# Optimization experiments

Hardware: AMD Instinct MI355X
Metric: run time of the kernel (lower is better)

Reference implementation:

```python
import jax, jax.numpy as jnp
import numpy as np

B, N, D_VIS, D_LBL = 64, 256, 2048, 512
H, F_OUT = 8, 256            # n_heads, gat_out_per_head_dim
D_IN = D_VIS + D_LBL         # 2560, GAT input dim
D_GAT = H * F_OUT            # 2048, concat-heads output dim
D_EMB = 512                  # final_embedding_dim
ALPHA = 0.2                  # LeakyReLU negative slope


def setup_inputs() -> dict:
    key = jax.random.key(0)
    ks = jax.random.split(key, 9)
    visual_features = jax.random.normal(ks[0], (B, D_VIS), jnp.float32)
    labels_features = jax.random.normal(ks[1], (N, D_LBL), jnp.float32)
    adj = (jax.random.uniform(ks[2], (N, N)) < 0.1).astype(jnp.float32)
    label_adj_matrix = jnp.maximum(adj, jnp.eye(N, dtype=jnp.float32))
    s = 1.0 / np.sqrt(D_IN)
    W_gat = jax.random.uniform(ks[3], (D_IN, H, F_OUT), jnp.float32, -s, s)
    a_src = jax.random.uniform(ks[4], (H, F_OUT), jnp.float32, -s, s)
    a_dst = jax.random.uniform(ks[5], (H, F_OUT), jnp.float32, -s, s)
    sg = 1.0 / np.sqrt(D_GAT)
    pool_q = jax.random.uniform(ks[6], (D_GAT,), jnp.float32, -sg, sg)
    fc_W = jax.random.uniform(ks[7], (D_GAT, D_EMB), jnp.float32, -sg, sg)
    fc_b = jax.random.uniform(ks[8], (D_EMB,), jnp.float32, -sg, sg)
    return {"visual_features": visual_features, "labels_features": labels_features,
            "label_adj_matrix": label_adj_matrix, "W_gat": W_gat, "a_src": a_src,
            "a_dst": a_dst, "pool_q": pool_q, "fc_W": fc_W, "fc_b": fc_b}


def reference(visual_features, labels_features, label_adj_matrix,
              W_gat, a_src, a_dst, pool_q, fc_W, fc_b):
    # Build per-sample contextualized label node features: (B, N, D_IN)
    x = jnp.concatenate(
        [jnp.broadcast_to(labels_features[None], (B, N, D_LBL)),
         jnp.broadcast_to(visual_features[:, None, :], (B, N, D_VIS))], axis=-1)
    # Multi-head GAT layer, batched over B (the torch code loops over B)
    Wh = jnp.einsum('bnd,dhf->bnhf', x, W_gat)            # (B, N, H, F)
    src = jnp.einsum('bnhf,hf->bhn', Wh, a_src)           # (B, H, N)
    dst = jnp.einsum('bnhf,hf->bhn', Wh, a_dst)           # (B, H, N)
    e = src[:, :, :, None] + dst[:, :, None, :]           # (B, H, N, N)
    e = jnp.where(e > 0, e, ALPHA * e)                    # LeakyReLU
    mask = (label_adj_matrix > 0)[None, None]             # (1, 1, N, N)
    scores = jnp.where(mask, e, jnp.float32(-9e15))
    attn = jax.nn.softmax(scores, axis=-1)                # (B, H, N, N)
    out = jnp.einsum('bhij,bjhf->bihf', attn, Wh)         # (B, N, H, F)
    out = jax.nn.elu(out.reshape(B, N, D_GAT))            # concat heads + ELU
    # attention pooling over label nodes
    pw = jax.nn.softmax(jnp.einsum('bnd,d->bn', out, pool_q), axis=-1)
    pooled = jnp.einsum('bn,bnd->bd', pw, out)            # (B, D_GAT)
    return pooled @ fc_W + fc_b                           # (B, D_EMB)
```

## Files before the change

kernel.cpp:

```cpp
#include <hip/hip_runtime.h>
#include <hip/hip_bf16.h>
#include <math.h>

#define BB 64
#define NN 256
#define D_VIS 2048
#define D_LBL 512
#define HH 8
#define FF 256
#define DG 2048
#define DE 512
#define ALPHA 0.2f
#define PSTRIDE 264
#define NSPLIT 4

using bf16 = __hip_bfloat16;
using short8 = __attribute__((ext_vector_type(8))) short;
using f32x4  = __attribute__((ext_vector_type(4))) float;
__device__ __forceinline__ float b2f(bf16 x) { return __bfloat162float(x); }
__device__ __forceinline__ unsigned short f2bs(float x) {
    bf16 h = __float2bfloat16(x);
    unsigned short u;
    __builtin_memcpy(&u, &h, 2);
    return u;
}
__device__ __forceinline__ float bs2f(unsigned short u) {
    unsigned int x = (unsigned int)u << 16;
    float f;
    __builtin_memcpy(&f, &x, 4);
    return f;
}

__global__ void __launch_bounds__(256) k_wh(const float* __restrict__ labels,
                                            const float* __restrict__ visual,
                                            const float* __restrict__ Wg,
                                            unsigned short* __restrict__ WhLbT,
                                            float* __restrict__ WhVz,
                                            const float* __restrict__ aSrc,
                                            const float* __restrict__ aDst,
                                            float* __restrict__ srcLp,
                                            float* __restrict__ dstLp,
                                            float* __restrict__ srcVp,
                                            float* __restrict__ dstVp,
                                            const float* __restrict__ adj,
                                            unsigned short* __restrict__ abits) {
    const int t = threadIdx.x;
    const int y = blockIdx.y;
    if (y == 8) {
        if (t < 128) {
            const int r = t >> 4, s = t & 15;
            const int i = blockIdx.x * 8 + r;
            unsigned int bits = 0;
#pragma unroll
            for (int jj = 0; jj < 8; ++jj) {
                const float2 av = *(const float2*)(adj + (size_t)i * NN + 2 * s + 32 * jj);
                bits |= (av.x > 0.f ? 1u : 0u) << (2 * jj);
                bits |= (av.y > 0.f ? 1u : 0u) << (2 * jj + 1);
            }
            abits[i * 16 + s] = (unsigned short)bits;
        }
        return;
    }

    __shared__ unsigned short As[2][64][72];
    __shared__ unsigned short Bs[2][64][72];
    const int w = t >> 6;
    const int lane = t & 63;
    const int l15 = lane & 15, quad = lane >> 4;
    const int n0 = blockIdx.x * 64;
    const int p2 = blockIdx.x & 3;
    const bool isL = (y < 4);
    const int m0  = isL ? y * 64 : 0;
    const int z   = isL ? 0 : (y - 4);
    const int kb0 = z * 512;
    const float* A = isL ? labels : visual;
    const int lda  = isL ? D_LBL : D_VIS;
    const float* Wb = Wg + (isL ? 0 : (size_t)D_LBL * DG);

    f32x4 acc[4];
#pragma unroll
    for (int mi = 0; mi < 4; ++mi) acc[mi] = (f32x4){0.f, 0.f, 0.f, 0.f};

    float4 ra[4], rb[4];
    auto load_tile = [&](int kc) {
        const int kb = kb0 + kc * 64;
#pragma unroll
        for (int p = 0; p < 4; ++p) {
            const int idx = t + 256 * p;
            const int r = idx >> 4, q4 = idx & 15;
            ra[p] = *(const float4*)(A + (size_t)(m0 + r) * lda + kb + 4 * q4);
        }
#pragma unroll
        for (int p = 0; p < 4; ++p) {
            const int kk = (t >> 4) + 16 * p;
            const int c4 = (t & 15) * 4;
            rb[p] = *(const float4*)(Wb + (size_t)(kb + kk) * DG + n0 + c4);
        }
    };
    auto store_tile = [&](int buf) {
#pragma unroll
        for (int p = 0; p < 4; ++p) {
            const int idx = t + 256 * p;
            const int r = idx >> 4, q4 = idx & 15;
            unsigned short s4[4] = {f2bs(ra[p].x), f2bs(ra[p].y), f2bs(ra[p].z), f2bs(ra[p].w)};
            __builtin_memcpy(&As[buf][r][4 * q4], s4, 8);
        }
#pragma unroll
        for (int p = 0; p < 4; ++p) {
            const int kk = (t >> 4) + 16 * p;
            const int c4 = (t & 15) * 4;
            Bs[buf][c4 + 0][kk] = f2bs(rb[p].x);
            Bs[buf][c4 + 1][kk] = f2bs(rb[p].y);
            Bs[buf][c4 + 2][kk] = f2bs(rb[p].z);
            Bs[buf][c4 + 3][kk] = f2bs(rb[p].w);
        }
    };

    load_tile(0);
    store_tile(0);
    __syncthreads();
    for (int kc = 0; kc < 8; ++kc) {
        const int cur = kc & 1;
        if (kc < 7) load_tile(kc + 1);
#pragma unroll
        for (int ks = 0; ks < 2; ++ks) {
            const short8 bf = *(const short8*)&Bs[cur][w * 16 + l15][ks * 32 + quad * 8];
#pragma unroll
            for (int mi = 0; mi < 4; ++mi) {
                const short8 af = *(const short8*)&As[cur][mi * 16 + l15][ks * 32 + quad * 8];
                acc[mi] = __builtin_amdgcn_mfma_f32_16x16x32_bf16(af, bf, acc[mi], 0, 0, 0);
            }
        }
        if (kc < 7) store_tile(cur ^ 1);
        __syncthreads();
    }
    const int col = n0 + w * 16 + l15;
    const int h = col >> 8;
    const float as = aSrc[col], ad = aDst[col];
    if (isL) {
#pragma unroll
        for (int mi = 0; mi < 4; ++mi) {
            unsigned short s4[4];
#pragma unroll
            for (int r = 0; r < 4; ++r) s4[r] = f2bs(acc[mi][r]);
            __builtin_memcpy(&WhLbT[(size_t)col * NN + m0 + mi * 16 + quad * 4], s4, 8);
        }
#pragma unroll
        for (int mi = 0; mi < 4; ++mi)
#pragma unroll
            for (int r = 0; r < 4; ++r) {
                float sv = acc[mi][r] * as;
                float dv = acc[mi][r] * ad;
#pragma unroll
                for (int off = 1; off < 16; off <<= 1) {
                    sv += __shfl_xor(sv, off);
                    dv += __shfl_xor(dv, off);
                }
                if (l15 == 0) {
                    const int row = m0 + mi * 16 + quad * 4 + r;
                    srcLp[(p2 * NN + row) * HH + h] = sv;
                    dstLp[(p2 * NN + row) * HH + h] = dv;
                }
            }
    } else {
        float* Wv = WhVz + (size_t)z * BB * DG;
#pragma unroll
        for (int mi = 0; mi < 4; ++mi)
#pragma unroll
            for (int r = 0; r < 4; ++r)
                Wv[(size_t)(mi * 16 + quad * 4 + r) * DG + col] = acc[mi][r];
        const int pv = p2 * 4 + z;
#pragma unroll
        for (int mi = 0; mi < 4; ++mi)
#pragma unroll
            for (int r = 0; r < 4; ++r) {
                float sv = acc[mi][r] * as;
                float dv = acc[mi][r] * ad;
#pragma unroll
                for (int off = 1; off < 16; off <<= 1) {
                    sv += __shfl_xor(sv, off);
                    dv += __shfl_xor(dv, off);
                }
                if (l15 == 0) {
                    const int row = mi * 16 + quad * 4 + r;
                    srcVp[(pv * BB + row) * HH + h] = sv;
                    dstVp[(pv * BB + row) * HH + h] = dv;
                }
            }
    }
}

__global__ void __launch_bounds__(512, 4) k_gat(const unsigned short* __restrict__ WhLbT,
                                                const float* __restrict__ WhVz,
                                                const float* __restrict__ srcLp,
                                                const float* __restrict__ dstLp,
                                                const float* __restrict__ srcVp,
                                                const float* __restrict__ dstVp,
                                                const unsigned short* __restrict__ abits,
                                                const float* __restrict__ pool_q,
                                                bf16* __restrict__ outb,
                                                float* __restrict__ ps_p) {
    const int bid = blockIdx.x;
    const int h = bid & 7;
    const int b = bid >> 3;
    const int t = threadIdx.x;
    const int w = t >> 6;
    const int lane = t & 63;
    const int l15 = lane & 15, quad = lane >> 4;

    __shared__ __align__(16) unsigned short Pl[64][PSTRIDE];
    __shared__ __align__(16) float dls2[2 * NN];
    __shared__ float slsA[NN], slsC[NN], slsTE[NN];
    __shared__ float inv[64];
    __shared__ float psl[8][64];

    if (t < NN) {
        float dl = 0.f, sl = 0.f;
#pragma unroll
        for (int p = 0; p < 4; ++p) {
            dl += dstLp[(p * NN + t) * HH + h];
            sl += srcLp[(p * NN + t) * HH + h];
        }
        dls2[2 * t]     = __expf(dl);
        dls2[2 * t + 1] = __expf(ALPHA * dl);
        float c = 0.f;
#pragma unroll
        for (int p = 0; p < 16; ++p)
            c += srcVp[(p * BB + b) * HH + h] + dstVp[(p * BB + b) * HH + h];
        const float u = c + sl;
        slsA[t]  = __expf(u);
        slsC[t]  = __expf(ALPHA * u);
        slsTE[t] = __expf(-u);
    }
    const int n0 = w * 32;
    float wv[2] = {0.f, 0.f};
#pragma unroll
    for (int z = 0; z < 4; ++z)
#pragma unroll
        for (int ni = 0; ni < 2; ++ni)
            wv[ni] += WhVz[(size_t)z * BB * DG + (size_t)b * DG + h * FF + n0 + ni * 16 + l15];
    const float pqv0 = pool_q[h * FF + n0 + l15];
    const float pqv1 = pool_q[h * FF + n0 + 16 + l15];
    const unsigned short* wb = WhLbT + (size_t)(h * FF + n0 + l15) * NN + quad * 8;
    __syncthreads();

    for (int it = 0; it < 4; ++it) {
        const int i0 = it * 64;

        {
            const int g = lane >> 4, s = lane & 15;
#pragma unroll
            for (int rr = 0; rr < 2; ++rr) {
                const int iloc = w * 8 + rr * 4 + g;
                const int i = i0 + iloc;
                const unsigned int mb = abits[i * 16 + s];
                const float Ai = slsA[i], Ci = slsC[i], TEi = slsTE[i];
                float pr[16];
                float sum = 0.f;
#pragma unroll
                for (int jj = 0; jj < 8; ++jj) {
                    const int j0 = 2 * s + 32 * jj;
                    const float4 bd = *(const float4*)&dls2[2 * j0];
                    const bool g0 = bd.x > TEi;
                    const bool g1 = bd.z > TEi;
                    float p0 = (g0 ? Ai : Ci) * (g0 ? bd.x : bd.y);
                    float p1 = (g1 ? Ai : Ci) * (g1 ? bd.z : bd.w);
                    p0 = (mb & (1u << (2 * jj)))     ? p0 : 0.f;
                    p1 = (mb & (1u << (2 * jj + 1))) ? p1 : 0.f;
                    pr[2 * jj] = p0; pr[2 * jj + 1] = p1;
                    sum += p0 + p1;
                }
#pragma unroll
                for (int off = 1; off < 16; off <<= 1) sum += __shfl_xor(sum, off);
                if (s == 0) inv[iloc] = 1.0f / sum;
#pragma unroll
                for (int jj = 0; jj < 8; ++jj) {
                    const unsigned int pk =
                        ((unsigned int)f2bs(pr[2 * jj + 1]) << 16) | f2bs(pr[2 * jj]);
                    *(unsigned int*)&Pl[iloc][2 * s + 32 * jj] = pk;
                }
            }
        }
        __syncthreads();

        f32x4 acc[4][2];
#pragma unroll
        for (int mi = 0; mi < 4; ++mi)
#pragma unroll
            for (int ni = 0; ni < 2; ++ni) acc[mi][ni] = (f32x4){0.f, 0.f, 0.f, 0.f};

        short8 bc0 = *(const short8*)(wb);
        short8 bc1 = *(const short8*)(wb + (size_t)16 * NN);
#pragma unroll
        for (int kc = 0; kc < 8; ++kc) {
            short8 bn0, bn1;
            if (kc < 7) {
                bn0 = *(const short8*)(wb + (kc + 1) * 32);
                bn1 = *(const short8*)(wb + (size_t)16 * NN + (kc + 1) * 32);
            }
            short8 a[4];
#pragma unroll
            for (int mi = 0; mi < 4; ++mi)
                a[mi] = *(const short8*)&Pl[mi * 16 + l15][kc * 32 + quad * 8];
#pragma unroll
            for (int mi = 0; mi < 4; ++mi)
                acc[mi][0] = __builtin_amdgcn_mfma_f32_16x16x32_bf16(a[mi], bc0, acc[mi][0], 0, 0, 0);
#pragma unroll
            for (int mi = 0; mi < 4; ++mi)
                acc[mi][1] = __builtin_amdgcn_mfma_f32_16x16x32_bf16(a[mi], bc1, acc[mi][1], 0, 0, 0);
            bc0 = bn0; bc1 = bn1;
        }

#pragma unroll
        for (int mi = 0; mi < 4; ++mi)
#pragma unroll
            for (int r = 0; r < 4; ++r) {
                const int row = mi * 16 + quad * 4 + r;
                const float ivr = inv[row];
                bf16* orow = outb + ((size_t)(b * NN + i0 + row)) * DG + h * FF + n0;
                float x0 = fmaf(acc[mi][0][r], ivr, wv[0]);
                float x1 = fmaf(acc[mi][1][r], ivr, wv[1]);
                x0 = x0 > 0.f ? x0 : (__expf(x0) - 1.0f);
                x1 = x1 > 0.f ? x1 : (__expf(x1) - 1.0f);
                orow[l15]      = __float2bfloat16(x0);
                orow[16 + l15] = __float2bfloat16(x1);
                float dot = fmaf(x0, pqv0, x1 * pqv1);
#pragma unroll
                for (int off = 1; off < 16; off <<= 1) dot += __shfl_xor(dot, off);
                if (l15 == 0) psl[w][row] = dot;
            }
        __syncthreads();
        if (t < 64) {
            float s = 0.f;
#pragma unroll
            for (int ww = 0; ww < 8; ++ww) s += psl[ww][t];
            ps_p[((size_t)h * BB + b) * NN + i0 + t] = s;
        }
    }
}

__global__ void __launch_bounds__(256) k_pool(const bf16* __restrict__ outb,
                                              const float* __restrict__ ps_p,
                                              float* __restrict__ pooled_p,
                                              const float* __restrict__ fcb,
                                              float* __restrict__ out) {
    const int dt = blockIdx.x;
    const int b  = blockIdx.y;
    const int ns = blockIdx.z;
    const int t  = threadIdx.x;
    if (dt == 0 && ns == 0) {
        out[b * DE + t]       = fcb[t];
        out[b * DE + 256 + t] = fcb[256 + t];
    }
    __shared__ float wsm[NN];
    __shared__ float redm[4];
    __shared__ float reds[4];
    float v = 0.f;
#pragma unroll
    for (int s = 0; s < 8; ++s)
        v += ps_p[((size_t)s * BB + b) * NN + t];
    float m = v;
#pragma unroll
    for (int off = 32; off; off >>= 1) m = fmaxf(m, __shfl_xor(m, off));
    if ((t & 63) == 0) redm[t >> 6] = m;
    __syncthreads();
    m = fmaxf(fmaxf(redm[0], redm[1]), fmaxf(redm[2], redm[3]));
    const float e = __expf(v - m);
    float s = e;
#pragma unroll
    for (int off = 32; off; off >>= 1) s += __shfl_xor(s, off);
    if ((t & 63) == 0) reds[t >> 6] = s;
    __syncthreads();
    s = reds[0] + reds[1] + reds[2] + reds[3];
    wsm[t] = e / s;
    __syncthreads();
    const int d0 = dt * 512 + t * 2;
    const int nb = ns * 64;
    float a0 = 0.f, a1 = 0.f;
    const bf16* base = outb + (size_t)b * NN * DG + d0;
#pragma unroll 8
    for (int n = 0; n < 64; ++n) {
        unsigned int q = *(const unsigned int*)(base + (size_t)(nb + n) * DG);
        const float wn = wsm[nb + n];
        a0 = fmaf(wn, bs2f((unsigned short)(q & 0xffff)), a0);
        a1 = fmaf(wn, bs2f((unsigned short)(q >> 16)), a1);
    }
    float2 r2 = {a0, a1};
    *(float2*)(pooled_p + ((size_t)(ns * BB + b)) * DG + d0) = r2;
}

__global__ void __launch_bounds__(256) k_mgemm(const float* __restrict__ Ap,
                                               const float* __restrict__ W, int ldw,
                                               float* __restrict__ C, int ldc,
                                               int kSlice, int kIters) {
    __shared__ unsigned short As[32][72];
    __shared__ unsigned short Bs[64][72];
    const int t = threadIdx.x;
    const int w = t >> 6;
    const int lane = t & 63;
    const int l15 = lane & 15, quad = lane >> 4;
    const int n0 = blockIdx.x * 64;
    const int m0 = blockIdx.y * 32;
    const int kb0 = blockIdx.z * kSlice;
    f32x4 acc[2];
    acc[0] = (f32x4){0.f, 0.f, 0.f, 0.f};
    acc[1] = (f32x4){0.f, 0.f, 0.f, 0.f};
    for (int kc = 0; kc < kIters; ++kc) {
        const int kb = kb0 + kc * 64;
#pragma unroll
        for (int p = 0; p < 2; ++p) {
            const int idx = t + 256 * p;
            const int r = idx >> 4, q4 = idx & 15;
            const float* ap = Ap + (size_t)(m0 + r) * DG + kb + 4 * q4;
            const float4 v0 = *(const float4*)(ap);
            const float4 v1 = *(const float4*)(ap + (size_t)BB * DG);
            const float4 v2 = *(const float4*)(ap + (size_t)2 * BB * DG);
            const float4 v3 = *(const float4*)(ap + (size_t)3 * BB * DG);
            const float vx = v0.x + v1.x + v2.x + v3.x;
            const float vy = v0.y + v1.y + v2.y + v3.y;
            const float vz = v0.z + v1.z + v2.z + v3.z;
            const float vw = v0.w + v1.w + v2.w + v3.w;
            unsigned short s4[4] = {f2bs(vx), f2bs(vy), f2bs(vz), f2bs(vw)};
            __builtin_memcpy(&As[r][4 * q4], s4, 8);
        }
#pragma unroll
        for (int p = 0; p < 4; ++p) {
            const int kk = (t >> 4) + 16 * p;
            const int c4 = (t & 15) * 4;
            const float4 v = *(const float4*)(W + (size_t)(kb + kk) * ldw + n0 + c4);
            Bs[c4 + 0][kk] = f2bs(v.x);
            Bs[c4 + 1][kk] = f2bs(v.y);
            Bs[c4 + 2][kk] = f2bs(v.z);
            Bs[c4 + 3][kk] = f2bs(v.w);
        }
        __syncthreads();
#pragma unroll
        for (int ks = 0; ks < 2; ++ks) {
            const short8 bf = *(const short8*)&Bs[w * 16 + l15][ks * 32 + quad * 8];
#pragma unroll
            for (int mi = 0; mi < 2; ++mi) {
                const short8 af = *(const short8*)&As[mi * 16 + l15][ks * 32 + quad * 8];
                acc[mi] = __builtin_amdgcn_mfma_f32_16x16x32_bf16(af, bf, acc[mi], 0, 0, 0);
            }
        }
        __syncthreads();
    }
    const int col = n0 + w * 16 + l15;
#pragma unroll
    for (int mi = 0; mi < 2; ++mi)
#pragma unroll
        for (int r = 0; r < 4; ++r)
            atomicAdd(&C[(size_t)(m0 + mi * 16 + quad * 4 + r) * ldc + col], acc[mi][r]);
}

extern "C" void kernel_launch(void* const* d_in, const int* in_sizes, int n_in,
                              void* d_out, int out_size, void* d_ws, size_t ws_size,
                              hipStream_t stream) {
    (void)in_sizes; (void)n_in; (void)out_size; (void)ws_size;
    const float* visual = (const float*)d_in[0];
    const float* labels = (const float*)d_in[1];
    const float* adj    = (const float*)d_in[2];
    const float* Wg     = (const float*)d_in[3];
    const float* a_src  = (const float*)d_in[4];
    const float* a_dst  = (const float*)d_in[5];
    const float* pool_q = (const float*)d_in[6];
    const float* fcW    = (const float*)d_in[7];
    const float* fcb    = (const float*)d_in[8];
    float* out = (float*)d_out;

    float* ws_f     = (float*)d_ws;
    float* WhVz     = ws_f;
    float* srcLp    = WhVz + 4 * BB * DG;
    float* dstLp    = srcLp + 4 * NN * HH;
    float* srcVp    = dstLp + 4 * NN * HH;
    float* dstVp    = srcVp + 16 * BB * HH;
    float* ps_p     = dstVp + 16 * BB * HH;
    float* pooled_p = ps_p + 8 * BB * NN;
    bf16*  outb     = (bf16*)(pooled_p + NSPLIT * BB * DG);
    unsigned short* WhLbT = (unsigned short*)(outb + (size_t)BB * NN * DG);
    unsigned short* abits = WhLbT + (size_t)DG * NN;

    k_wh<<<dim3(DG / 64, 9), 256, 0, stream>>>(labels, visual, Wg, WhLbT, WhVz,
                                               a_src, a_dst, srcLp, dstLp, srcVp, dstVp,
                                               adj, abits);

    k_gat<<<BB * HH, 512, 0, stream>>>(WhLbT, WhVz, srcLp, dstLp, srcVp, dstVp,
                                       abits, pool_q, outb, ps_p);

    k_pool<<<dim3(4, BB, NSPLIT), 256, 0, stream>>>(outb, ps_p, pooled_p, fcb, out);

    k_mgemm<<<dim3(DE / 64, BB / 32, 16), 256, 0, stream>>>(
        pooled_p, fcW, DE, out, DE, 128, 2);
}
```

Before: 165.5 us.

## Split Wh GEMM finer, reorder grid by role, widen pooling loads

The labels GEMM now uses 32-row tiles (8 blocks) and the visual GEMM splits K eight ways instead of four. The grid is reordered so that role is the fast index, which gives 17x32 blocks and more parallelism in the first kernel. The pooling kernel reads 8 bf16 values per thread in 16-byte loads over 32-node slices with NSPLIT=8, and the final GEMM sums the extra partials. In exchange there are more partial buffers to write and reduce in the later kernels.

Measured after the change: 175.2 us. 1.06x slower.

```diff
diff --git a/kernel.cpp b/kernel.cpp
--- a/kernel.cpp
+++ b/kernel.cpp
@@ -12,7 +12,7 @@
 #define DE 512
 #define ALPHA 0.2f
 #define PSTRIDE 264
-#define NSPLIT 4
+#define NSPLIT 8
 
 using bf16 = __hip_bfloat16;
 using short8 = __attribute__((ext_vector_type(8))) short;
@@ -45,11 +45,12 @@
                                             const float* __restrict__ adj,
                                             unsigned short* __restrict__ abits) {
     const int t = threadIdx.x;
-    const int y = blockIdx.y;
-    if (y == 8) {
+    const int role = blockIdx.x;
+    const int bx = blockIdx.y;
+    if (role == 16) {
         if (t < 128) {
             const int r = t >> 4, s = t & 15;
-            const int i = blockIdx.x * 8 + r;
+            const int i = bx * 8 + r;
             unsigned int bits = 0;
 #pragma unroll
             for (int jj = 0; jj < 8; ++jj) {
@@ -67,86 +68,79 @@
     const int w = t >> 6;
     const int lane = t & 63;
     const int l15 = lane & 15, quad = lane >> 4;
-    const int n0 = blockIdx.x * 64;
-    const int p2 = blockIdx.x & 3;
-    const bool isL = (y < 4);
-    const int m0  = isL ? y * 64 : 0;
-    const int z   = isL ? 0 : (y - 4);
-    const int kb0 = z * 512;
-    const float* A = isL ? labels : visual;
-    const int lda  = isL ? D_LBL : D_VIS;
-    const float* Wb = Wg + (isL ? 0 : (size_t)D_LBL * DG);
-
-    f32x4 acc[4];
-#pragma unroll
-    for (int mi = 0; mi < 4; ++mi) acc[mi] = (f32x4){0.f, 0.f, 0.f, 0.f};
-
-    float4 ra[4], rb[4];
-    auto load_tile = [&](int kc) {
-        const int kb = kb0 + kc * 64;
-#pragma unroll
-        for (int p = 0; p < 4; ++p) {
-            const int idx = t + 256 * p;
-            const int r = idx >> 4, q4 = idx & 15;
-            ra[p] = *(const float4*)(A + (size_t)(m0 + r) * lda + kb + 4 * q4);
-        }
-#pragma unroll
-        for (int p = 0; p < 4; ++p) {
-            const int kk = (t >> 4) + 16 * p;
-            const int c4 = (t & 15) * 4;
-            rb[p] = *(const float4*)(Wb + (size_t)(kb + kk) * DG + n0 + c4);
-        }
-    };
-    auto store_tile = [&](int buf) {
-#pragma unroll
-        for (int p = 0; p < 4; ++p) {
-            const int idx = t + 256 * p;
-            const int r = idx >> 4, q4 = idx & 15;
-            unsigned short s4[4] = {f2bs(ra[p].x), f2bs(ra[p].y), f2bs(ra[p].z), f2bs(ra[p].w)};
-            __builtin_memcpy(&As[buf][r][4 * q4], s4, 8);
-        }
-#pragma unroll
-        for (int p = 0; p < 4; ++p) {
-            const int kk = (t >> 4) + 16 * p;
-            const int c4 = (t & 15) * 4;
-            Bs[buf][c4 + 0][kk] = f2bs(rb[p].x);
-            Bs[buf][c4 + 1][kk] = f2bs(rb[p].y);
-            Bs[buf][c4 + 2][kk] = f2bs(rb[p].z);
-            Bs[buf][c4 + 3][kk] = f2bs(rb[p].w);
-        }
-    };
-
-    load_tile(0);
-    store_tile(0);
-    __syncthreads();
-    for (int kc = 0; kc < 8; ++kc) {
-        const int cur = kc & 1;
-        if (kc < 7) load_tile(kc + 1);
-#pragma unroll
-        for (int ks = 0; ks < 2; ++ks) {
-            const short8 bf = *(const short8*)&Bs[cur][w * 16 + l15][ks * 32 + quad * 8];
-#pragma unroll
-            for (int mi = 0; mi < 4; ++mi) {
-                const short8 af = *(const short8*)&As[cur][mi * 16 + l15][ks * 32 + quad * 8];
-                acc[mi] = __builtin_amdgcn_mfma_f32_16x16x32_bf16(af, bf, acc[mi], 0, 0, 0);
-            }
-        }
-        if (kc < 7) store_tile(cur ^ 1);
-        __syncthreads();
-    }
+    const int n0 = bx * 64;
+    const int p2 = bx & 3;
+    const bool isL = (role < 8);
     const int col = n0 + w * 16 + l15;
     const int h = col >> 8;
     const float as = aSrc[col], ad = aDst[col];
+
     if (isL) {
-#pragma unroll
-        for (int mi = 0; mi < 4; ++mi) {
+        const int m0 = role * 32;
+        f32x4 acc[2];
+        acc[0] = (f32x4){0.f, 0.f, 0.f, 0.f};
+        acc[1] = (f32x4){0.f, 0.f, 0.f, 0.f};
+        float4 ra[2], rb[4];
+        auto load_tile = [&](int kc) {
+            const int kb = kc * 64;
+#pragma unroll
+            for (int p = 0; p < 2; ++p) {
+                const int idx = t + 256 * p;
+                const int r = idx >> 4, q4 = idx & 15;
+                ra[p] = *(const float4*)(labels + (size_t)(m0 + r) * D_LBL + kb + 4 * q4);
+            }
+#pragma unroll
+            for (int p = 0; p < 4; ++p) {
+                const int kk = (t >> 4) + 16 * p;
+                const int c4 = (t & 15) * 4;
+                rb[p] = *(const float4*)(Wg + (size_t)(kb + kk) * DG + n0 + c4);
+            }
+        };
+        auto store_tile = [&](int buf) {
+#pragma unroll
+            for (int p = 0; p < 2; ++p) {
+                const int idx = t + 256 * p;
+                const int r = idx >> 4, q4 = idx & 15;
+                unsigned short s4[4] = {f2bs(ra[p].x), f2bs(ra[p].y), f2bs(ra[p].z), f2bs(ra[p].w)};
+                __builtin_memcpy(&As[buf][r][4 * q4], s4, 8);
+            }
+#pragma unroll
+            for (int p = 0; p < 4; ++p) {
+                const int kk = (t >> 4) + 16 * p;
+                const int c4 = (t & 15) * 4;
+                Bs[buf][c4 + 0][kk] = f2bs(rb[p].x);
+                Bs[buf][c4 + 1][kk] = f2bs(rb[p].y);
+                Bs[buf][c4 + 2][kk] = f2bs(rb[p].z);
+                Bs[buf][c4 + 3][kk] = f2bs(rb[p].w);
+            }
+        };
+        load_tile(0);
+        store_tile(0);
+        __syncthreads();
+        for (int kc = 0; kc < 8; ++kc) {
+            const int cur = kc & 1;
+            if (kc < 7) load_tile(kc + 1);
+#pragma unroll
+            for (int ks = 0; ks < 2; ++ks) {
+                const short8 bf = *(const short8*)&Bs[cur][w * 16 + l15][ks * 32 + quad * 8];
+#pragma unroll
+                for (int mi = 0; mi < 2; ++mi) {
+                    const short8 af = *(const short8*)&As[cur][mi * 16 + l15][ks * 32 + quad * 8];
+                    acc[mi] = __builtin_amdgcn_mfma_f32_16x16x32_bf16(af, bf, acc[mi], 0, 0, 0);
+                }
+            }
+            if (kc < 7) store_tile(cur ^ 1);
+            __syncthreads();
+        }
+#pragma unroll
+        for (int mi = 0; mi < 2; ++mi) {
             unsigned short s4[4];
 #pragma unroll
             for (int r = 0; r < 4; ++r) s4[r] = f2bs(acc[mi][r]);
             __builtin_memcpy(&WhLbT[(size_t)col * NN + m0 + mi * 16 + quad * 4], s4, 8);
         }
 #pragma unroll
-        for (int mi = 0; mi < 4; ++mi)
+        for (int mi = 0; mi < 2; ++mi)
 #pragma unroll
             for (int r = 0; r < 4; ++r) {
                 float sv = acc[mi][r] * as;
@@ -163,13 +157,71 @@
                 }
             }
     } else {
+        const int z = role - 8;
+        const int kb0 = z * 256;
+        const float* Wb = Wg + (size_t)D_LBL * DG;
+        f32x4 acc[4];
+#pragma unroll
+        for (int mi = 0; mi < 4; ++mi) acc[mi] = (f32x4){0.f, 0.f, 0.f, 0.f};
+        float4 ra[4], rb[4];
+        auto load_tile = [&](int kc) {
+            const int kb = kb0 + kc * 64;
+#pragma unroll
+            for (int p = 0; p < 4; ++p) {
+                const int idx = t + 256 * p;
+                const int r = idx >> 4, q4 = idx & 15;
+                ra[p] = *(const float4*)(visual + (size_t)r * D_VIS + kb + 4 * q4);
+            }
+#pragma unroll
+            for (int p = 0; p < 4; ++p) {
+                const int kk = (t >> 4) + 16 * p;
+                const int c4 = (t & 15) * 4;
+                rb[p] = *(const float4*)(Wb + (size_t)(kb + kk) * DG + n0 + c4);
+            }
+        };
+        auto store_tile = [&](int buf) {
+#pragma unroll
+            for (int p = 0; p < 4; ++p) {
+                const int idx = t + 256 * p;
+                const int r = idx >> 4, q4 = idx & 15;
+                unsigned short s4[4] = {f2bs(ra[p].x), f2bs(ra[p].y), f2bs(ra[p].z), f2bs(ra[p].w)};
+                __builtin_memcpy(&As[buf][r][4 * q4], s4, 8);
+            }
+#pragma unroll
+            for (int p = 0; p < 4; ++p) {
+                const int kk = (t >> 4) + 16 * p;
+                const int c4 = (t & 15) * 4;
+                Bs[buf][c4 + 0][kk] = f2bs(rb[p].x);
+                Bs[buf][c4 + 1][kk] = f2bs(rb[p].y);
+                Bs[buf][c4 + 2][kk] = f2bs(rb[p].z);
+                Bs[buf][c4 + 3][kk] = f2bs(rb[p].w);
+            }
+        };
+        load_tile(0);
+        store_tile(0);
+        __syncthreads();
+        for (int kc = 0; kc < 4; ++kc) {
+            const int cur = kc & 1;
+            if (kc < 3) load_tile(kc + 1);
+#pragma unroll
+            for (int ks = 0; ks < 2; ++ks) {
+                const short8 bf = *(const short8*)&Bs[cur][w * 16 + l15][ks * 32 + quad * 8];
+#pragma unroll
+                for (int mi = 0; mi < 4; ++mi) {
+                    const short8 af = *(const short8*)&As[cur][mi * 16 + l15][ks * 32 + quad * 8];
+                    acc[mi] = __builtin_amdgcn_mfma_f32_16x16x32_bf16(af, bf, acc[mi], 0, 0, 0);
+                }
+            }
+            if (kc < 3) store_tile(cur ^ 1);
+            __syncthreads();
+        }
         float* Wv = WhVz + (size_t)z * BB * DG;
 #pragma unroll
         for (int mi = 0; mi < 4; ++mi)
 #pragma unroll
             for (int r = 0; r < 4; ++r)
                 Wv[(size_t)(mi * 16 + quad * 4 + r) * DG + col] = acc[mi][r];
-        const int pv = p2 * 4 + z;
+        const int pv = p2 * 8 + z;
 #pragma unroll
         for (int mi = 0; mi < 4; ++mi)
 #pragma unroll
@@ -225,7 +277,7 @@
         dls2[2 * t + 1] = __expf(ALPHA * dl);
         float c = 0.f;
 #pragma unroll
-        for (int p = 0; p < 16; ++p)
+        for (int p = 0; p < 32; ++p)
             c += srcVp[(p * BB + b) * HH + h] + dstVp[(p * BB + b) * HH + h];
         const float u = c + sl;
         slsA[t]  = __expf(u);
@@ -235,7 +287,7 @@
     const int n0 = w * 32;
     float wv[2] = {0.f, 0.f};
 #pragma unroll
-    for (int z = 0; z < 4; ++z)
+    for (int z = 0; z < 8; ++z)
 #pragma unroll
         for (int ni = 0; ni < 2; ++ni)
             wv[ni] += WhVz[(size_t)z * BB * DG + (size_t)b * DG + h * FF + n0 + ni * 16 + l15];
@@ -344,11 +396,10 @@
                                               float* __restrict__ pooled_p,
                                               const float* __restrict__ fcb,
                                               float* __restrict__ out) {
-    const int dt = blockIdx.x;
-    const int b  = blockIdx.y;
-    const int ns = blockIdx.z;
+    const int b  = blockIdx.x;
+    const int ns = blockIdx.y;
     const int t  = threadIdx.x;
-    if (dt == 0 && ns == 0) {
+    if (ns == 0) {
         out[b * DE + t]       = fcb[t];
         out[b * DE + 256 + t] = fcb[256 + t];
     }
@@ -374,19 +425,25 @@
     s = reds[0] + reds[1] + reds[2] + reds[3];
     wsm[t] = e / s;
     __syncthreads();
-    const int d0 = dt * 512 + t * 2;
-    const int nb = ns * 64;
-    float a0 = 0.f, a1 = 0.f;
+    const int d0 = t * 8;
+    const int nb = ns * 32;
+    float a[8];
+#pragma unroll
+    for (int j = 0; j < 8; ++j) a[j] = 0.f;
     const bf16* base = outb + (size_t)b * NN * DG + d0;
-#pragma unroll 8
-    for (int n = 0; n < 64; ++n) {
-        unsigned int q = *(const unsigned int*)(base + (size_t)(nb + n) * DG);
+#pragma unroll 4
+    for (int n = 0; n < 32; ++n) {
+        const short8 q = *(const short8*)(base + (size_t)(nb + n) * DG);
         const float wn = wsm[nb + n];
-        a0 = fmaf(wn, bs2f((unsigned short)(q & 0xffff)), a0);
-        a1 = fmaf(wn, bs2f((unsigned short)(q >> 16)), a1);
-    }
-    float2 r2 = {a0, a1};
-    *(float2*)(pooled_p + ((size_t)(ns * BB + b)) * DG + d0) = r2;
+#pragma unroll
+        for (int j = 0; j < 8; ++j)
+            a[j] = fmaf(wn, bs2f((unsigned short)q[j]), a[j]);
+    }
+    float* pp = pooled_p + ((size_t)ns * BB + b) * DG + d0;
+    float4 r0 = {a[0], a[1], a[2], a[3]};
+    float4 r1 = {a[4], a[5], a[6], a[7]};
+    *(float4*)pp = r0;
+    *(float4*)(pp + 4) = r1;
 }
 
 __global__ void __launch_bounds__(256) k_mgemm(const float* __restrict__ Ap,
@@ -412,15 +469,13 @@
             const int idx = t + 256 * p;
             const int r = idx >> 4, q4 = idx & 15;
             const float* ap = Ap + (size_t)(m0 + r) * DG + kb + 4 * q4;
-            const float4 v0 = *(const float4*)(ap);
-            const float4 v1 = *(const float4*)(ap + (size_t)BB * DG);
-            const float4 v2 = *(const float4*)(ap + (size_t)2 * BB * DG);
-            const float4 v3 = *(const float4*)(ap + (size_t)3 * BB * DG);
-            const float vx = v0.x + v1.x + v2.x + v3.x;
-            const float vy = v0.y + v1.y + v2.y + v3.y;
-            const float vz = v0.z + v1.z + v2.z + v3.z;
-            const float vw = v0.w + v1.w + v2.w + v3.w;
-            unsigned short s4[4] = {f2bs(vx), f2bs(vy), f2bs(vz), f2bs(vw)};
+            float4 vs = *(const float4*)ap;
+#pragma unroll
+            for (int s2 = 1; s2 < NSPLIT; ++s2) {
+                const float4 vv = *(const float4*)(ap + (size_t)s2 * BB * DG);
+                vs.x += vv.x; vs.y += vv.y; vs.z += vv.z; vs.w += vv.w;
+            }
+            unsigned short s4[4] = {f2bs(vs.x), f2bs(vs.y), f2bs(vs.z), f2bs(vs.w)};
             __builtin_memcpy(&As[r][4 * q4], s4, 8);
         }
 #pragma unroll
@@ -470,24 +525,24 @@
 
     float* ws_f     = (float*)d_ws;
     float* WhVz     = ws_f;
-    float* srcLp    = WhVz + 4 * BB * DG;
+    float* srcLp    = WhVz + 8 * BB * DG;
     float* dstLp    = srcLp + 4 * NN * HH;
     float* srcVp    = dstLp + 4 * NN * HH;
-    float* dstVp    = srcVp + 16 * BB * HH;
-    float* ps_p     = dstVp + 16 * BB * HH;
+    float* dstVp    = srcVp + 32 * BB * HH;
+    float* ps_p     = dstVp + 32 * BB * HH;
     float* pooled_p = ps_p + 8 * BB * NN;
     bf16*  outb     = (bf16*)(pooled_p + NSPLIT * BB * DG);
     unsigned short* WhLbT = (unsigned short*)(outb + (size_t)BB * NN * DG);
     unsigned short* abits = WhLbT + (size_t)DG * NN;
 
-    k_wh<<<dim3(DG / 64, 9), 256, 0, stream>>>(labels, visual, Wg, WhLbT, WhVz,
-                                               a_src, a_dst, srcLp, dstLp, srcVp, dstVp,
-                                               adj, abits);
+    k_wh<<<dim3(17, 32), 256, 0, stream>>>(labels, visual, Wg, WhLbT, WhVz,
+                                           a_src, a_dst, srcLp, dstLp, srcVp, dstVp,
+                                           adj, abits);
 
     k_gat<<<BB * HH, 512, 0, stream>>>(WhLbT, WhVz, srcLp, dstLp, srcVp, dstVp,
                                        abits, pool_q, outb, ps_p);
 
-    k_pool<<<dim3(4, BB, NSPLIT), 256, 0, stream>>>(outb, ps_p, pooled_p, fcb, out);
+    k_pool<<<dim3(BB, NSPLIT), 256, 0, stream>>>(outb, ps_p, pooled_p, fcb, out);
 
     k_mgemm<<<dim3(DE / 64, BB / 32, 16), 256, 0, stream>>>(
         pooled_p, fcW, DE, out, DE, 128, 2);
```
